# Kernel optimization log

Measured on AMD Instinct MI355X. Metric: run time of the kernel, lower is better.

Reference implementation:

```python
import jax, jax.numpy as jnp
import numpy as np

N_HEAD, D_EMB, D_MLP, D_HEAD = 12, 768, 3072, 64
LN_EPS = 1e-5


def setup_inputs() -> dict:
    key = jax.random.key(0)
    ks = jax.random.split(key, 12)
    s = 0.02
    return {
        "x": jax.random.normal(ks[0], (2, 4096, D_EMB), dtype=jnp.float32),
        "ln1_g": jnp.ones((D_EMB,), jnp.float32),
        "ln1_b": jnp.zeros((D_EMB,), jnp.float32),
        "wqkv_w": jax.random.normal(ks[1], (D_EMB, 3 * D_EMB), jnp.float32) * s,
        "wo_w": jax.random.normal(ks[2], (D_EMB, D_EMB), jnp.float32) * s,
        "wo_b": jnp.zeros((D_EMB,), jnp.float32),
        "ln2_g": jnp.ones((D_EMB,), jnp.float32),
        "ln2_b": jnp.zeros((D_EMB,), jnp.float32),
        "w1_w": jax.random.normal(ks[3], (D_EMB, D_MLP), jnp.float32) * s,
        "w1_b": jnp.zeros((D_MLP,), jnp.float32),
        "w2_w": jax.random.normal(ks[4], (D_MLP, D_EMB), jnp.float32) * s,
        "w2_b": jnp.zeros((D_EMB,), jnp.float32),
    }


def _layernorm(x, g, b):
    mu = jnp.mean(x, axis=-1, keepdims=True)
    var = jnp.var(x, axis=-1, keepdims=True)
    return (x - mu) * jax.lax.rsqrt(var + LN_EPS) * g + b


def _attn(x, wqkv_w, wo_w, wo_b):
    B, T, d = x.shape
    qkv = x @ wqkv_w  # [B,T,3d]
    q, k, v = jnp.split(qkv, 3, axis=-1)
    q = q.reshape(B, T, N_HEAD, D_HEAD).transpose(0, 2, 1, 3)  # [B,H,T,dh]
    k = k.reshape(B, T, N_HEAD, D_HEAD).transpose(0, 2, 1, 3)
    v = v.reshape(B, T, N_HEAD, D_HEAD).transpose(0, 2, 1, 3)
    A = jnp.einsum('bhqd,bhkd->bhqk', q, k) / np.sqrt(D_HEAD).astype(np.float32)
    mask = jnp.tril(jnp.ones((T, T), dtype=bool))
    A = jnp.where(mask, A, -jnp.inf)
    A = jax.nn.softmax(A - jax.lax.stop_gradient(jnp.max(A, axis=-1, keepdims=True)), axis=-1)
    y = jnp.einsum('bhqk,bhkd->bhqd', A, v)  # [B,H,T,dh]
    y = y.transpose(0, 2, 1, 3).reshape(B, T, d)
    return y @ wo_w + wo_b


def _mlp(x, w1_w, w1_b, w2_w, w2_b):
    h = jax.nn.gelu(x @ w1_w + w1_b, approximate=False)
    return h @ w2_w + w2_b


def reference(x, ln1_g, ln1_b, wqkv_w, wo_w, wo_b, ln2_g, ln2_b, w1_w, w1_b, w2_w, w2_b):
    x = x + _attn(_layernorm(x, ln1_g, ln1_b), wqkv_w, wo_w, wo_b)
    x = x + _mlp(_layernorm(x, ln2_g, ln2_b), w1_w, w1_b, w2_w, w2_b)
    return x
```

## Files before the change

kernel.cpp:

```cpp
#include <hip/hip_runtime.h>

#define T_SEQ 4096
#define D_EMB 768
#define N_HEAD 12
#define D_HEAD 64
#define D_MLP 3072
#define NTOK 8192
#define QSCALE 0.18033688011112043f

typedef __bf16 v8bf __attribute__((ext_vector_type(8)));
typedef float v4f __attribute__((ext_vector_type(4)));

template <int N> struct IC { static constexpr int value = N; };

__device__ __forceinline__ unsigned short f2bf(float f) {
    unsigned int u = __float_as_uint(f);
    unsigned int r = (u + 0x7fffu + ((u >> 16) & 1u)) >> 16;
    return (unsigned short)r;
}

__device__ __forceinline__ void g2lds16(const void* g, void* l) {
    __builtin_amdgcn_global_load_lds(
        (const __attribute__((address_space(1))) void*)g,
        (__attribute__((address_space(3))) void*)l, 16, 0, 0);
}

__global__ void tcast_kernel(const float* __restrict__ in, unsigned short* __restrict__ out,
                             int K, int N) {
    __shared__ float tile[32][33];
    int k0 = blockIdx.y * 32, n0 = blockIdx.x * 32;
    int tx = threadIdx.x, ty = threadIdx.y;
    for (int i = ty; i < 32; i += 8)
        tile[i][tx] = in[(size_t)(k0 + i) * N + n0 + tx];
    __syncthreads();
    for (int i = ty; i < 32; i += 8)
        out[(size_t)(n0 + i) * K + k0 + tx] = f2bf(tile[tx][i]);
}

__global__ void vtrans_kernel(const unsigned short* __restrict__ in,
                              unsigned short* __restrict__ out) {
    __shared__ unsigned short tile[32][33];
    size_t base = (size_t)blockIdx.z * T_SEQ * D_HEAD;
    int t0 = blockIdx.x * 32, d0 = blockIdx.y * 32;
    int tx = threadIdx.x, ty = threadIdx.y;
    for (int i = ty; i < 32; i += 8)
        tile[i][tx] = in[base + (size_t)(t0 + i) * D_HEAD + d0 + tx];
    __syncthreads();
    size_t tbase = base + (size_t)(t0 >> 6) * 4096 + (t0 & 32);
    for (int i = ty; i < 32; i += 8)
        out[tbase + (size_t)(d0 + i) * 64 + tx] = tile[tx][i];
}

__global__ __launch_bounds__(256) void ln_kernel(const float* __restrict__ x,
                                                 const float* __restrict__ g,
                                                 const float* __restrict__ bta,
                                                 unsigned short* __restrict__ out) {
    int row = blockIdx.x;
    const float* xr = x + (size_t)row * D_EMB;
    int tid = threadIdx.x;
    float v[3];
    float s = 0.f, s2 = 0.f;
#pragma unroll
    for (int i = 0; i < 3; i++) {
        v[i] = xr[tid + i * 256];
        s += v[i];
        s2 += v[i] * v[i];
    }
#pragma unroll
    for (int o = 1; o < 64; o <<= 1) {
        s += __shfl_xor(s, o);
        s2 += __shfl_xor(s2, o);
    }
    __shared__ float red[8];
    int wave = tid >> 6, lane = tid & 63;
    if (lane == 0) { red[wave] = s; red[wave + 4] = s2; }
    __syncthreads();
    s = red[0] + red[1] + red[2] + red[3];
    s2 = red[4] + red[5] + red[6] + red[7];
    float mu = s * (1.f / 768.f);
    float var = s2 * (1.f / 768.f) - mu * mu;
    float rstd = rsqrtf(var + 1e-5f);
#pragma unroll
    for (int i = 0; i < 3; i++) {
        int c = tid + i * 256;
        out[(size_t)row * D_EMB + c] = f2bf((v[i] - mu) * rstd * g[c] + bta[c]);
    }
}

template <int EPI>
__global__ __launch_bounds__(256) void gemm_kernel(
    const unsigned short* __restrict__ A, const unsigned short* __restrict__ Bt, int K,
    int Nt, const float* __restrict__ bias, const float* __restrict__ resid,
    float* __restrict__ outF, unsigned short* __restrict__ outB,
    unsigned short* __restrict__ Qb, unsigned short* __restrict__ Kb,
    unsigned short* __restrict__ Vb) {
    __shared__ unsigned short As[2][4096];
    __shared__ unsigned short Bs[2][4096];
    const int tid = threadIdx.x;
    const int wave = tid >> 6, lane = tid & 63;
    const int wm = wave >> 1, wn = wave & 1;
    const int n16 = lane & 15, kq = lane >> 4;
    const int id = blockIdx.x;
    const int xcd = id & 7, s = id >> 3;
    const int mt = xcd * 8 + s / Nt, nt_ = s % Nt;
    const long m0 = (long)mt * 128, nb0 = (long)nt_ * 128;

    const int c0 = (wave * 2 + 0) * 64 + lane;
    const int c1 = (wave * 2 + 1) * 64 + lane;
    const unsigned short* aP0 = A + (m0 + (c0 >> 2)) * K + ((c0 & 3) << 3);
    const unsigned short* aP1 = A + (m0 + (c1 >> 2)) * K + ((c1 & 3) << 3);
    const unsigned short* bP0 = Bt + (nb0 + (c0 >> 2)) * K + ((c0 & 3) << 3);
    const unsigned short* bP1 = Bt + (nb0 + (c1 >> 2)) * K + ((c1 & 3) << 3);
    const int fw = (wn * 64 + n16) * 32 + kq * 8;
    const int fa = (wm * 64 + n16) * 32 + kq * 8;

    const v4f vzero = {0.f, 0.f, 0.f, 0.f};
    v4f acc[4][4];
#pragma unroll
    for (int wi = 0; wi < 4; wi++)
#pragma unroll
        for (int ai = 0; ai < 4; ai++) acc[wi][ai] = vzero;

    auto stage = [&](auto BUFC, int kpos) {
        constexpr int nb = decltype(BUFC)::value;
        g2lds16(aP0 + kpos, &As[nb][(wave * 2 + 0) * 512]);
        g2lds16(aP1 + kpos, &As[nb][(wave * 2 + 1) * 512]);
        g2lds16(bP0 + kpos, &Bs[nb][(wave * 2 + 0) * 512]);
        g2lds16(bP1 + kpos, &Bs[nb][(wave * 2 + 1) * 512]);
    };
    auto gstep = [&](auto BUFC, int kpos, bool pref) {
        constexpr int buf = decltype(BUFC)::value;
        __syncthreads();
        if (pref) stage(IC<buf ^ 1>{}, kpos + 32);
        v8bf wf[4], af[4];
#pragma unroll
        for (int i = 0; i < 4; i++) {
            wf[i] = *(const v8bf*)(&Bs[buf][fw + i * 512]);
            af[i] = *(const v8bf*)(&As[buf][fa + i * 512]);
        }
#pragma unroll
        for (int wi = 0; wi < 4; wi++)
#pragma unroll
            for (int ai = 0; ai < 4; ai++)
                acc[wi][ai] = __builtin_amdgcn_mfma_f32_16x16x32_bf16(wf[wi], af[ai],
                                                                     acc[wi][ai], 0, 0, 0);
    };

    stage(IC<0>{}, 0);
#pragma unroll 1
    for (int k0 = 0; k0 < K; k0 += 64) {
        gstep(IC<0>{}, k0, true);
        gstep(IC<1>{}, k0 + 32, k0 + 64 < K);
    }

#pragma unroll
    for (int wi = 0; wi < 4; wi++) {
#pragma unroll
        for (int ai = 0; ai < 4; ai++) {
            const long Nb = nb0 + wn * 64 + wi * 16 + kq * 4;
            const long M = m0 + wm * 64 + ai * 16 + n16;
            if (EPI == 0) {
                int which = (int)(Nb / 768);
                int c = (int)(Nb - which * 768);
                int hh = c >> 6, ii = c & 63;
                int bb = (int)(M >> 12), t = (int)(M & 4095);
                size_t dst = (((size_t)bb * N_HEAD + hh) * T_SEQ + t) * D_HEAD + ii;
                union { uint2 u2; unsigned short us[4]; } pk;
#pragma unroll
                for (int r = 0; r < 4; r++) {
                    float v = acc[wi][ai][r];
                    if (which == 0) v *= QSCALE;
                    pk.us[r] = f2bf(v);
                }
                if (which == 0) *(uint2*)(&Qb[dst]) = pk.u2;
                else if (which == 1) *(uint2*)(&Kb[dst]) = pk.u2;
                else *(uint2*)(&Vb[dst]) = pk.u2;
            } else if (EPI == 1) {
                float4 b4 = *(const float4*)(&bias[Nb]);
                float4 r4 = *(const float4*)(&resid[M * 768 + Nb]);
                float4 o4;
                o4.x = acc[wi][ai][0] + b4.x + r4.x;
                o4.y = acc[wi][ai][1] + b4.y + r4.y;
                o4.z = acc[wi][ai][2] + b4.z + r4.z;
                o4.w = acc[wi][ai][3] + b4.w + r4.w;
                *(float4*)(&outF[M * 768 + Nb]) = o4;
            } else {
                float4 b4 = *(const float4*)(&bias[Nb]);
                union { uint2 u2; unsigned short us[4]; } pk;
#pragma unroll
                for (int r = 0; r < 4; r++) {
                    float t = acc[wi][ai][r] + ((const float*)&b4)[r];
                    pk.us[r] = f2bf(0.5f * t * (1.f + erff(t * 0.70710678118f)));
                }
                *(uint2*)(&outB[M * 3072 + Nb]) = pk.u2;
            }
        }
    }
}

#define PSTR 72
__global__ __launch_bounds__(256) void attn_kernel(const unsigned short* __restrict__ Q,
                                                   const unsigned short* __restrict__ Kg,
                                                   const unsigned short* __restrict__ Vt,
                                                   unsigned short* __restrict__ y) {
    __shared__ unsigned short Kt[2][4096];
    __shared__ unsigned short Vl[2][4096];
    __shared__ unsigned short Ps[4 * 16 * PSTR];
    const int tid = threadIdx.x;
    const int wave = tid >> 6, lane = tid & 63;
    const int n16 = lane & 15, kq = lane >> 4;
    const int id = blockIdx.x;
    const int xcd = id & 7, slot = id >> 3;
    const int combo = xcd * 3 + (slot >> 5);
    const int pair = slot & 31;
    const int h = combo % N_HEAD, b = combo / N_HEAD;
    const size_t hoff = (((size_t)b * N_HEAD + h) * T_SEQ) * D_HEAD;
    const unsigned short* Qh = Q + hoff;
    const unsigned short* Kh = Kg + hoff;
    const unsigned short* Vh = Vt + hoff;
    const v4f vzero = {0.f, 0.f, 0.f, 0.f};

    const int sC0 = (wave * 2 + 0) * 64 + lane;
    const int sC1 = (wave * 2 + 1) * 64 + lane;
    const int soff0 = (sC0 >> 3) * 64 + ((((sC0 & 7) ^ ((sC0 >> 3) & 7))) << 3);
    const int soff1 = (sC1 >> 3) * 64 + ((((sC1 & 7) ^ ((sC1 >> 3) & 7))) << 3);
    const int fb0 = n16 * 64 + (((0 * 4 + kq) ^ (n16 & 7)) << 3);
    const int fb1 = n16 * 64 + (((1 * 4 + kq) ^ (n16 & 7)) << 3);
    unsigned short* pwr = &Ps[wave * 1152 + n16 * PSTR + kq * 4];
    const unsigned short* prd = &Ps[wave * 1152 + n16 * PSTR + kq * 8];
    v8bf vone;
#pragma unroll
    for (int j = 0; j < 8; j++) ((unsigned short*)&vone)[j] = 0x3F80;

    const unsigned short* knext;
    const unsigned short* vnext;
    v4f o[4], lacc;
    int qt, qglob;
    v8bf qf[2];

    auto step = [&](auto BUFC, int kt, bool pref, bool diag) {
        constexpr int buf = decltype(BUFC)::value;
        __syncthreads();
        if (pref) {
            g2lds16(knext + soff0, &Kt[buf ^ 1][(wave * 2 + 0) * 512]);
            g2lds16(knext + soff1, &Kt[buf ^ 1][(wave * 2 + 1) * 512]);
            g2lds16(vnext + soff0, &Vl[buf ^ 1][(wave * 2 + 0) * 512]);
            g2lds16(vnext + soff1, &Vl[buf ^ 1][(wave * 2 + 1) * 512]);
            knext += 4096;
            vnext += 4096;
        }
        v4f s[4];
#pragma unroll
        for (int nt = 0; nt < 4; nt++) s[nt] = vzero;
#pragma unroll
        for (int nt = 0; nt < 4; nt++) {
            v8bf k0 = *(const v8bf*)(&Kt[buf][nt * 1024 + fb0]);
            v8bf k1 = *(const v8bf*)(&Kt[buf][nt * 1024 + fb1]);
            s[nt] = __builtin_amdgcn_mfma_f32_16x16x32_bf16(k0, qf[0], s[nt], 0, 0, 0);
            s[nt] = __builtin_amdgcn_mfma_f32_16x16x32_bf16(k1, qf[1], s[nt], 0, 0, 0);
        }
#pragma unroll
        for (int nt = 0; nt < 4; nt++) {
            union { uint2 u2; __bf16 hh[4]; } pk;
#pragma unroll
            for (int r = 0; r < 4; r++) {
                float p = __builtin_amdgcn_exp2f(s[nt][r]);
                if (diag) {
                    int key = kt * 64 + nt * 16 + kq * 4 + r;
                    if (key > qglob) p = 0.f;
                }
                pk.hh[r] = (__bf16)p;
            }
            *(uint2*)(&pwr[nt * 16]) = pk.u2;
        }
#pragma unroll
        for (int ks = 0; ks < 2; ks++) {
            v8bf pa = *(const v8bf*)(&prd[ks * 32]);
            lacc = __builtin_amdgcn_mfma_f32_16x16x32_bf16(pa, vone, lacc, 0, 0, 0);
#pragma unroll
            for (int nt = 0; nt < 4; nt++) {
                v8bf vb = *(const v8bf*)(&Vl[buf][nt * 1024 + (ks ? fb1 : fb0)]);
                o[nt] = __builtin_amdgcn_mfma_f32_16x16x32_bf16(pa, vb, o[nt], 0, 0, 0);
            }
        }
    };

#pragma unroll 1
    for (int half = 0; half < 2; half++) {
        qt = half ? (63 - pair) : pair;
        qglob = qt * 64 + wave * 16 + n16;
#pragma unroll
        for (int ks = 0; ks < 2; ks++)
            qf[ks] = *(const v8bf*)(&Qh[(size_t)qglob * D_HEAD + ks * 32 + kq * 8]);
#pragma unroll
        for (int nt = 0; nt < 4; nt++) o[nt] = vzero;
        lacc = vzero;

        __syncthreads();
        const unsigned short* kb = Kh + (size_t)0;
        const unsigned short* vb_ = Vh + (size_t)0;
        g2lds16(kb + soff0, &Kt[0][(wave * 2 + 0) * 512]);
        g2lds16(kb + soff1, &Kt[0][(wave * 2 + 1) * 512]);
        g2lds16(vb_ + soff0, &Vl[0][(wave * 2 + 0) * 512]);
        g2lds16(vb_ + soff1, &Vl[0][(wave * 2 + 1) * 512]);
        knext = Kh + 4096;
        vnext = Vh + 4096;

        int kt = 0;
#pragma unroll 1
        while (kt + 2 <= qt) {
            step(IC<0>{}, kt, true, false);
            step(IC<1>{}, kt + 1, true, false);
            kt += 2;
        }
        if (kt < qt) {
            step(IC<0>{}, kt, true, false);
            step(IC<1>{}, kt + 1, false, true);
        } else {
            step(IC<0>{}, kt, false, true);
        }

        float linv[4];
#pragma unroll
        for (int r = 0; r < 4; r++) linv[r] = 1.f / lacc[r];
#pragma unroll
        for (int nt = 0; nt < 4; nt++)
#pragma unroll
            for (int r = 0; r < 4; r++) {
                int q = qt * 64 + wave * 16 + kq * 4 + r;
                float val = o[nt][r] * linv[r];
                y[((size_t)b * T_SEQ + q) * D_EMB + h * 64 + nt * 16 + n16] = f2bf(val);
            }
    }
}

extern "C" void kernel_launch(void* const* d_in, const int* in_sizes, int n_in,
                              void* d_out, int out_size, void* d_ws, size_t ws_size,
                              hipStream_t stream) {
    const float* x = (const float*)d_in[0];
    const float* ln1_g = (const float*)d_in[1];
    const float* ln1_b = (const float*)d_in[2];
    const float* wqkv_w = (const float*)d_in[3];
    const float* wo_w = (const float*)d_in[4];
    const float* wo_b = (const float*)d_in[5];
    const float* ln2_g = (const float*)d_in[6];
    const float* ln2_b = (const float*)d_in[7];
    const float* w1_w = (const float*)d_in[8];
    const float* w1_b = (const float*)d_in[9];
    const float* w2_w = (const float*)d_in[10];
    const float* w2_b = (const float*)d_in[11];
    float* out = (float*)d_out;

    char* ws = (char*)d_ws;
    size_t off = 0;
    auto alloc = [&](size_t bytes) -> void* {
        void* p = ws + off;
        off += (bytes + 255) & ~(size_t)255;
        return p;
    };
    unsigned short* xn = (unsigned short*)alloc((size_t)NTOK * D_EMB * 2);
    unsigned short* wqkvT = (unsigned short*)alloc((size_t)2304 * 768 * 2);
    unsigned short* woT = (unsigned short*)alloc((size_t)768 * 768 * 2);
    unsigned short* w1T = (unsigned short*)alloc((size_t)3072 * 768 * 2);
    unsigned short* w2T = (unsigned short*)alloc((size_t)768 * 3072 * 2);
    unsigned short* Qb = (unsigned short*)alloc((size_t)NTOK * D_EMB * 2);
    unsigned short* Kb = (unsigned short*)alloc((size_t)NTOK * D_EMB * 2);
    unsigned short* Vb = (unsigned short*)alloc((size_t)NTOK * D_EMB * 2);
    unsigned short* yb = (unsigned short*)alloc((size_t)NTOK * D_EMB * 2);
    float* res1 = (float*)alloc((size_t)NTOK * D_EMB * 4);
    unsigned short* Vtb = xn;
    unsigned short* hbuf = Qb;

    dim3 tb(32, 8);
    tcast_kernel<<<dim3(2304 / 32, 768 / 32), tb, 0, stream>>>(wqkv_w, wqkvT, 768, 2304);
    tcast_kernel<<<dim3(768 / 32, 768 / 32), tb, 0, stream>>>(wo_w, woT, 768, 768);
    tcast_kernel<<<dim3(3072 / 32, 768 / 32), tb, 0, stream>>>(w1_w, w1T, 768, 3072);
    tcast_kernel<<<dim3(768 / 32, 3072 / 32), tb, 0, stream>>>(w2_w, w2T, 3072, 768);

    ln_kernel<<<NTOK, 256, 0, stream>>>(x, ln1_g, ln1_b, xn);

    gemm_kernel<0><<<64 * 18, 256, 0, stream>>>(
        xn, wqkvT, 768, 18, nullptr, nullptr, nullptr, nullptr, Qb, Kb, Vb);

    vtrans_kernel<<<dim3(T_SEQ / 32, 2, 2 * N_HEAD), tb, 0, stream>>>(Vb, Vtb);

    attn_kernel<<<768, 256, 0, stream>>>(Qb, Kb, Vtb, yb);

    gemm_kernel<1><<<64 * 6, 256, 0, stream>>>(
        yb, woT, 768, 6, wo_b, x, res1, nullptr, nullptr, nullptr, nullptr);

    ln_kernel<<<NTOK, 256, 0, stream>>>(res1, ln2_g, ln2_b, xn);

    gemm_kernel<2><<<64 * 24, 256, 0, stream>>>(
        xn, w1T, 768, 24, w1_b, nullptr, nullptr, hbuf, nullptr, nullptr, nullptr);

    gemm_kernel<1><<<64 * 6, 256, 0, stream>>>(
        hbuf, w2T, 3072, 6, w2_b, res1, out, nullptr, nullptr, nullptr, nullptr);
}
```

Before: 457.5 us.

## Process 128-query tiles per block with two 16-row groups per wave

Each attention block now handles a single 128-query tile, with each wave covering 32 query rows as two 16-row groups that share every loaded K/V tile. This replaces the earlier scheme of processing two paired 64-query tiles in sequence. Doubling the query rows per K/V load halves LDS K/V traffic per unit of work and removes the per-half reload and sync. In exchange, register pressure rises, and the causal load balance changes because block work now varies with j. Blocks are ordered largest-first.

```diff
diff --git a/kernel.cpp b/kernel.cpp
--- a/kernel.cpp
+++ b/kernel.cpp
@@ -205,14 +205,14 @@
                                                    unsigned short* __restrict__ y) {
     __shared__ unsigned short Kt[2][4096];
     __shared__ unsigned short Vl[2][4096];
-    __shared__ unsigned short Ps[4 * 16 * PSTR];
+    __shared__ unsigned short Ps[4][2][16 * PSTR];
     const int tid = threadIdx.x;
     const int wave = tid >> 6, lane = tid & 63;
     const int n16 = lane & 15, kq = lane >> 4;
     const int id = blockIdx.x;
     const int xcd = id & 7, slot = id >> 3;
     const int combo = xcd * 3 + (slot >> 5);
-    const int pair = slot & 31;
+    const int j = 31 - (slot & 31);
     const int h = combo % N_HEAD, b = combo / N_HEAD;
     const size_t hoff = (((size_t)b * N_HEAD + h) * T_SEQ) * D_HEAD;
     const unsigned short* Qh = Q + hoff;
@@ -224,19 +224,41 @@
     const int sC1 = (wave * 2 + 1) * 64 + lane;
     const int soff0 = (sC0 >> 3) * 64 + ((((sC0 & 7) ^ ((sC0 >> 3) & 7))) << 3);
     const int soff1 = (sC1 >> 3) * 64 + ((((sC1 & 7) ^ ((sC1 >> 3) & 7))) << 3);
-    const int fb0 = n16 * 64 + (((0 * 4 + kq) ^ (n16 & 7)) << 3);
-    const int fb1 = n16 * 64 + (((1 * 4 + kq) ^ (n16 & 7)) << 3);
-    unsigned short* pwr = &Ps[wave * 1152 + n16 * PSTR + kq * 4];
-    const unsigned short* prd = &Ps[wave * 1152 + n16 * PSTR + kq * 8];
+    const int fb0 = n16 * 64 + ((kq ^ (n16 & 7)) << 3);
+    const int fb1 = n16 * 64 + (((4 + kq) ^ (n16 & 7)) << 3);
+    unsigned short* pwr0 = &Ps[wave][0][n16 * PSTR + kq * 4];
+    unsigned short* pwr1 = &Ps[wave][1][n16 * PSTR + kq * 4];
+    const unsigned short* prd0 = &Ps[wave][0][n16 * PSTR + kq * 8];
+    const unsigned short* prd1 = &Ps[wave][1][n16 * PSTR + kq * 8];
     v8bf vone;
 #pragma unroll
-    for (int j = 0; j < 8; j++) ((unsigned short*)&vone)[j] = 0x3F80;
-
-    const unsigned short* knext;
-    const unsigned short* vnext;
-    v4f o[4], lacc;
-    int qt, qglob;
-    v8bf qf[2];
+    for (int jj = 0; jj < 8; jj++) ((unsigned short*)&vone)[jj] = 0x3F80;
+
+    const int nsteps = 2 * j + 2;
+    const int qg0 = j * 128 + wave * 32 + n16;
+    const int qg1 = qg0 + 16;
+    v8bf qf[2][2];
+#pragma unroll
+    for (int q16 = 0; q16 < 2; q16++)
+#pragma unroll
+        for (int ks = 0; ks < 2; ks++)
+            qf[q16][ks] = *(const v8bf*)(
+                &Qh[(size_t)(qg0 + q16 * 16) * D_HEAD + ks * 32 + kq * 8]);
+
+    v4f o[2][4], lacc[2];
+#pragma unroll
+    for (int q16 = 0; q16 < 2; q16++) {
+        lacc[q16] = vzero;
+#pragma unroll
+        for (int nt = 0; nt < 4; nt++) o[q16][nt] = vzero;
+    }
+
+    const unsigned short* knext = Kh + 4096;
+    const unsigned short* vnext = Vh + 4096;
+    g2lds16(Kh + soff0, &Kt[0][(wave * 2 + 0) * 512]);
+    g2lds16(Kh + soff1, &Kt[0][(wave * 2 + 1) * 512]);
+    g2lds16(Vh + soff0, &Vl[0][(wave * 2 + 0) * 512]);
+    g2lds16(Vh + soff1, &Vl[0][(wave * 2 + 1) * 512]);
 
     auto step = [&](auto BUFC, int kt, bool pref, bool diag) {
         constexpr int buf = decltype(BUFC)::value;
@@ -249,86 +271,68 @@
             knext += 4096;
             vnext += 4096;
         }
-        v4f s[4];
-#pragma unroll
-        for (int nt = 0; nt < 4; nt++) s[nt] = vzero;
-#pragma unroll
-        for (int nt = 0; nt < 4; nt++) {
-            v8bf k0 = *(const v8bf*)(&Kt[buf][nt * 1024 + fb0]);
-            v8bf k1 = *(const v8bf*)(&Kt[buf][nt * 1024 + fb1]);
-            s[nt] = __builtin_amdgcn_mfma_f32_16x16x32_bf16(k0, qf[0], s[nt], 0, 0, 0);
-            s[nt] = __builtin_amdgcn_mfma_f32_16x16x32_bf16(k1, qf[1], s[nt], 0, 0, 0);
+#pragma unroll
+        for (int q16 = 0; q16 < 2; q16++) {
+            v4f s[4];
+#pragma unroll
+            for (int nt = 0; nt < 4; nt++) s[nt] = vzero;
+#pragma unroll
+            for (int nt = 0; nt < 4; nt++) {
+                v8bf k0 = *(const v8bf*)(&Kt[buf][nt * 1024 + fb0]);
+                v8bf k1 = *(const v8bf*)(&Kt[buf][nt * 1024 + fb1]);
+                s[nt] = __builtin_amdgcn_mfma_f32_16x16x32_bf16(k0, qf[q16][0], s[nt], 0, 0, 0);
+                s[nt] = __builtin_amdgcn_mfma_f32_16x16x32_bf16(k1, qf[q16][1], s[nt], 0, 0, 0);
+            }
+            const int qg = q16 ? qg1 : qg0;
+            unsigned short* pw = q16 ? pwr1 : pwr0;
+#pragma unroll
+            for (int nt = 0; nt < 4; nt++) {
+                union { uint2 u2; __bf16 hh[4]; } pk;
+#pragma unroll
+                for (int r = 0; r < 4; r++) {
+                    float p = __builtin_amdgcn_exp2f(s[nt][r]);
+                    if (diag) {
+                        int key = kt * 64 + nt * 16 + kq * 4 + r;
+                        if (key > qg) p = 0.f;
+                    }
+                    pk.hh[r] = (__bf16)p;
+                }
+                *(uint2*)(&pw[nt * 16]) = pk.u2;
+            }
         }
 #pragma unroll
-        for (int nt = 0; nt < 4; nt++) {
-            union { uint2 u2; __bf16 hh[4]; } pk;
-#pragma unroll
-            for (int r = 0; r < 4; r++) {
-                float p = __builtin_amdgcn_exp2f(s[nt][r]);
-                if (diag) {
-                    int key = kt * 64 + nt * 16 + kq * 4 + r;
-                    if (key > qglob) p = 0.f;
-                }
-                pk.hh[r] = (__bf16)p;
-            }
-            *(uint2*)(&pwr[nt * 16]) = pk.u2;
-        }
-#pragma unroll
         for (int ks = 0; ks < 2; ks++) {
-            v8bf pa = *(const v8bf*)(&prd[ks * 32]);
-            lacc = __builtin_amdgcn_mfma_f32_16x16x32_bf16(pa, vone, lacc, 0, 0, 0);
+            v8bf pa0 = *(const v8bf*)(&prd0[ks * 32]);
+            v8bf pa1 = *(const v8bf*)(&prd1[ks * 32]);
+            lacc[0] = __builtin_amdgcn_mfma_f32_16x16x32_bf16(pa0, vone, lacc[0], 0, 0, 0);
+            lacc[1] = __builtin_amdgcn_mfma_f32_16x16x32_bf16(pa1, vone, lacc[1], 0, 0, 0);
 #pragma unroll
             for (int nt = 0; nt < 4; nt++) {
                 v8bf vb = *(const v8bf*)(&Vl[buf][nt * 1024 + (ks ? fb1 : fb0)]);
-                o[nt] = __builtin_amdgcn_mfma_f32_16x16x32_bf16(pa, vb, o[nt], 0, 0, 0);
+                o[0][nt] = __builtin_amdgcn_mfma_f32_16x16x32_bf16(pa0, vb, o[0][nt], 0, 0, 0);
+                o[1][nt] = __builtin_amdgcn_mfma_f32_16x16x32_bf16(pa1, vb, o[1][nt], 0, 0, 0);
             }
         }
     };
 
 #pragma unroll 1
-    for (int half = 0; half < 2; half++) {
-        qt = half ? (63 - pair) : pair;
-        qglob = qt * 64 + wave * 16 + n16;
-#pragma unroll
-        for (int ks = 0; ks < 2; ks++)
-            qf[ks] = *(const v8bf*)(&Qh[(size_t)qglob * D_HEAD + ks * 32 + kq * 8]);
-#pragma unroll
-        for (int nt = 0; nt < 4; nt++) o[nt] = vzero;
-        lacc = vzero;
-
-        __syncthreads();
-        const unsigned short* kb = Kh + (size_t)0;
-        const unsigned short* vb_ = Vh + (size_t)0;
-        g2lds16(kb + soff0, &Kt[0][(wave * 2 + 0) * 512]);
-        g2lds16(kb + soff1, &Kt[0][(wave * 2 + 1) * 512]);
-        g2lds16(vb_ + soff0, &Vl[0][(wave * 2 + 0) * 512]);
-        g2lds16(vb_ + soff1, &Vl[0][(wave * 2 + 1) * 512]);
-        knext = Kh + 4096;
-        vnext = Vh + 4096;
-
-        int kt = 0;
-#pragma unroll 1
-        while (kt + 2 <= qt) {
-            step(IC<0>{}, kt, true, false);
-            step(IC<1>{}, kt + 1, true, false);
-            kt += 2;
-        }
-        if (kt < qt) {
-            step(IC<0>{}, kt, true, false);
-            step(IC<1>{}, kt + 1, false, true);
-        } else {
-            step(IC<0>{}, kt, false, true);
-        }
-
+    for (int kt = 0; kt < nsteps; kt += 2) {
+        const bool lastp = (kt + 2 >= nsteps);
+        step(IC<0>{}, kt, true, lastp);
+        step(IC<1>{}, kt + 1, !lastp, lastp);
+    }
+
+#pragma unroll
+    for (int q16 = 0; q16 < 2; q16++) {
         float linv[4];
 #pragma unroll
-        for (int r = 0; r < 4; r++) linv[r] = 1.f / lacc[r];
+        for (int r = 0; r < 4; r++) linv[r] = 1.f / lacc[q16][r];
 #pragma unroll
         for (int nt = 0; nt < 4; nt++)
 #pragma unroll
             for (int r = 0; r < 4; r++) {
-                int q = qt * 64 + wave * 16 + kq * 4 + r;
-                float val = o[nt][r] * linv[r];
+                int q = j * 128 + wave * 32 + q16 * 16 + kq * 4 + r;
+                float val = o[q16][nt][r] * linv[r];
                 y[((size_t)b * T_SEQ + q) * D_EMB + h * 64 + nt * 16 + n16] = f2bf(val);
             }
     }
```

After: 478.5 us. 4.6% more time.
